# Kernel tuning notes

Measured on AMD Instinct MI355X. Metric: run time of the kernel, lower is better.

## Reference

```python
import jax, jax.numpy as jnp
import numpy as np

NV, NC = 100000, 50000        # num variables, num constraints
DV, DC = 8, 16                # padded neighbor-list widths
DIN, DH = 32, 128             # init_input_dim, output_dim (=init_output_dim)
NUM_LAYERS = 3                # aggregate loop runs num_layers-1 times
DCAT = 2 * DH + DIN           # input_dim of fc_variable/fc_constraint


def setup_inputs() -> dict:
    key = jax.random.key(0)
    ks = jax.random.split(key, 10)
    w = lambda k, shape: (jax.random.normal(k, shape, jnp.float32) * 0.05)
    return {
        "x": jax.random.normal(ks[0], (NV + NC, DIN), jnp.float32),
        "var_constr_index": jax.random.randint(ks[1], (NV, DV), 0, NC, dtype=jnp.int32),
        "constr_var_index": jax.random.randint(ks[2], (NC, DC), 0, NV, dtype=jnp.int32),
        "W_init_v": w(ks[3], (DIN, DH)), "b_init_v": jnp.zeros((DH,), jnp.float32),
        "W_init_c": w(ks[4], (DIN, DH)), "b_init_c": jnp.zeros((DH,), jnp.float32),
        "W_var": w(ks[5], (DCAT, DH)), "b_var": jnp.zeros((DH,), jnp.float32),
        "W_con": w(ks[6], (DCAT, DH)), "b_con": jnp.zeros((DH,), jnp.float32),
        "W_q": w(ks[7], (2 * DH, 1)), "b_q": jnp.zeros((1,), jnp.float32),
    }


def reference(x, var_constr_index, constr_var_index,
              W_init_v, b_init_v, W_init_c, b_init_c,
              W_var, b_var, W_con, b_con, W_q, b_q):
    nv = var_constr_index.shape[0]
    xv, xc = x[:nv], x[nv:]
    # layer zero init (fc_init_variables / fc_init_constraints)
    v = xv @ W_init_v + b_init_v          # [NV, DH]
    c = xc @ W_init_c + b_init_c          # [NC, DH]
    # message-passing layers: both updates read OLD v and OLD c
    for _ in range(1, NUM_LAYERS):
        agg_c = jnp.sum(v[constr_var_index], axis=1)   # [NC, DH] gather+sum over variable neighbors
        agg_v = jnp.sum(c[var_constr_index], axis=1)   # [NV, DH] gather+sum over constraint neighbors
        c_new = jnp.concatenate([agg_c, c, xc], axis=1) @ W_con + b_con
        v_new = jnp.concatenate([agg_v, v, xv], axis=1) @ W_var + b_var
        c, v = c_new, v_new
    # embedding_Q: global sum of variable features, broadcast, concat, linear
    g = jnp.sum(v, axis=0)                             # [DH]
    q_in = jnp.concatenate([jnp.broadcast_to(g, v.shape), v], axis=1)  # [NV, 2*DH]
    return q_in @ W_q + b_q                            # [NV, 1]
```

## Files before the change

kernel.cpp:

```cpp
#include <hip/hip_runtime.h>

#define NV 100000
#define NC 50000
#define DVAR 8
#define DCON 16

using short8 = __attribute__((ext_vector_type(8))) short;
using f32x4  = __attribute__((ext_vector_type(4))) float;

__device__ __forceinline__ unsigned short f2bf(float f) {
    union { float f; unsigned int u; } v; v.f = f;
    return (unsigned short)((v.u + 0x7fffu + ((v.u >> 16) & 1u)) >> 16);
}
__device__ __forceinline__ float bflo(unsigned int u) {
    union { unsigned int u; float f; } v; v.u = u << 16; return v.f;
}
__device__ __forceinline__ float bfhi(unsigned int u) {
    union { unsigned int u; float f; } v; v.u = u & 0xffff0000u; return v.f;
}

__global__ __launch_bounds__(256) void pack_kernel(
    const float* __restrict__ Wvar, const float* __restrict__ Wcon,
    const float* __restrict__ Wiv,  const float* __restrict__ Wic,
    unsigned short* __restrict__ WbVar, unsigned short* __restrict__ WbCon,
    unsigned short* __restrict__ WbIv,  unsigned short* __restrict__ WbIc,
    float* __restrict__ S)
{
    const int tid = blockIdx.x * 256 + threadIdx.x;
    for (int i = tid; i < 9 * 128 * 32; i += gridDim.x * 256) {
        int s = i >> 12, rem = i & 4095, c = rem >> 5, k = rem & 31;
        int src = (s * 32 + k) * 128 + c;
        WbVar[i] = f2bf(Wvar[src]);
        WbCon[i] = f2bf(Wcon[src]);
    }
    for (int i = tid; i < 128 * 32; i += gridDim.x * 256) {
        int c = i >> 5, k = i & 31;
        int src = k * 128 + c;
        WbIv[i] = f2bf(Wiv[src]);
        WbIc[i] = f2bf(Wic[src]);
    }
    if (tid == 0) S[0] = 0.f;
}

__global__ __launch_bounds__(256) void init_mfma(
    const float* __restrict__ x,
    const unsigned short* __restrict__ Wb,
    const float* __restrict__ bias,
    unsigned short* __restrict__ hout, int M)
{
    const int t = threadIdx.x;
    const int lane = t & 63;
    const int w = t >> 6;
    const int lrow = lane & 15;
    const int lg = lane >> 4;
    const int wrow0 = blockIdx.x * 64 + w * 16;
    int arow = wrow0 + lrow;
    int arowc = arow < M ? arow : M - 1;

    const float4* xp = (const float4*)(x + (size_t)arowc * 32 + lg * 8);
    float4 xa = xp[0], xb = xp[1];
    short8 afr;
    afr[0] = (short)f2bf(xa.x); afr[1] = (short)f2bf(xa.y);
    afr[2] = (short)f2bf(xa.z); afr[3] = (short)f2bf(xa.w);
    afr[4] = (short)f2bf(xb.x); afr[5] = (short)f2bf(xb.y);
    afr[6] = (short)f2bf(xb.z); afr[7] = (short)f2bf(xb.w);

    #pragma unroll
    for (int ct = 0; ct < 8; ++ct) {
        int c = ct * 16 + lrow;
        short8 bfr = *(const short8*)(Wb + (size_t)c * 32 + lg * 8);
        f32x4 acc = {0.f, 0.f, 0.f, 0.f};
        acc = __builtin_amdgcn_mfma_f32_16x16x32_bf16(afr, bfr, acc, 0, 0, 0);
        float bv = bias[c];
        #pragma unroll
        for (int r = 0; r < 4; ++r) {
            int orow = wrow0 + lg * 4 + r;
            if (orow < M) hout[(size_t)orow * 128 + c] = f2bf(acc[r] + bv);
        }
    }
}

template<int DEG>
__global__ __launch_bounds__(256) void agg_bf16(
    const unsigned short* __restrict__ hnb, const int* __restrict__ idx,
    unsigned short* __restrict__ agg, int M)
{
    const int tid = blockIdx.x * 256 + threadIdx.x;
    const int row = tid >> 4;
    const int part = tid & 15;
    if (row >= M) return;
    int nb[DEG];
    #pragma unroll
    for (int d4 = 0; d4 < DEG / 4; ++d4)
        *(int4*)(&nb[d4 * 4]) = *(const int4*)(idx + (size_t)row * DEG + d4 * 4);
    float a0=0.f,a1=0.f,a2=0.f,a3=0.f,a4=0.f,a5=0.f,a6=0.f,a7=0.f;
    #pragma unroll
    for (int b = 0; b < DEG; b += 8) {
        uint4 q[8];
        #pragma unroll
        for (int j = 0; j < 8; ++j)
            q[j] = *(const uint4*)(hnb + (size_t)nb[b + j] * 128 + part * 8);
        #pragma unroll
        for (int j = 0; j < 8; ++j) {
            a0 += bflo(q[j].x); a1 += bfhi(q[j].x);
            a2 += bflo(q[j].y); a3 += bfhi(q[j].y);
            a4 += bflo(q[j].z); a5 += bfhi(q[j].z);
            a6 += bflo(q[j].w); a7 += bfhi(q[j].w);
        }
    }
    uint4 o;
    o.x = (unsigned)f2bf(a0) | ((unsigned)f2bf(a1) << 16);
    o.y = (unsigned)f2bf(a2) | ((unsigned)f2bf(a3) << 16);
    o.z = (unsigned)f2bf(a4) | ((unsigned)f2bf(a5) << 16);
    o.w = (unsigned)f2bf(a6) | ((unsigned)f2bf(a7) << 16);
    *(uint4*)(agg + (size_t)row * 128 + part * 8) = o;
}

template<bool FINAL>
__global__ __launch_bounds__(256) void gemm_mfma(
    const unsigned short* hself,
    const unsigned short* __restrict__ aggin,
    const float* __restrict__ xself,
    const unsigned short* __restrict__ Wb,
    const float* __restrict__ bias,
    unsigned short* hout,
    const float* __restrict__ Wq, float* __restrict__ S, float* __restrict__ dotout,
    int M)
{
    __shared__ float red[4];
    const int t = threadIdx.x;
    const int lane = t & 63;
    const int w = t >> 6;
    const int lrow = lane & 15;
    const int lg = lane >> 4;
    const int wrow0 = blockIdx.x * 128 + w * 32;

    int arc[2];
    #pragma unroll
    for (int rt = 0; rt < 2; ++rt) {
        int r = wrow0 + rt * 16 + lrow;
        arc[rt] = r < M ? r : M - 1;
    }

    auto loadA = [&](int s, int rt) -> short8 {
        if (s < 4) {
            return *(const short8*)(aggin + (size_t)arc[rt] * 128 + s * 32 + lg * 8);
        } else if (s < 8) {
            return *(const short8*)(hself + (size_t)arc[rt] * 128 + (s - 4) * 32 + lg * 8);
        } else {
            const float4* xp = (const float4*)(xself + (size_t)arc[rt] * 32 + lg * 8);
            float4 xa = xp[0], xb = xp[1];
            short8 r8;
            r8[0] = (short)f2bf(xa.x); r8[1] = (short)f2bf(xa.y);
            r8[2] = (short)f2bf(xa.z); r8[3] = (short)f2bf(xa.w);
            r8[4] = (short)f2bf(xb.x); r8[5] = (short)f2bf(xb.y);
            r8[6] = (short)f2bf(xb.z); r8[7] = (short)f2bf(xb.w);
            return r8;
        }
    };

    short8 bfr[2][8];
    short8 afr[2][2];
    #pragma unroll
    for (int ct = 0; ct < 8; ++ct)
        bfr[0][ct] = *(const short8*)(Wb + ((size_t)(ct * 16 + lrow)) * 32 + lg * 8);
    afr[0][0] = loadA(0, 0);
    afr[0][1] = loadA(0, 1);

    f32x4 acc[2][8];
    #pragma unroll
    for (int rt = 0; rt < 2; ++rt)
        #pragma unroll
        for (int ct = 0; ct < 8; ++ct) acc[rt][ct] = (f32x4){0.f, 0.f, 0.f, 0.f};

    #pragma unroll
    for (int s = 0; s < 9; ++s) {
        const int cur = s & 1, nxt = cur ^ 1;
        if (s < 8) {
            #pragma unroll
            for (int ct = 0; ct < 8; ++ct)
                bfr[nxt][ct] = *(const short8*)(
                    Wb + ((size_t)(s + 1) * 128 + ct * 16 + lrow) * 32 + lg * 8);
            afr[nxt][0] = loadA(s + 1, 0);
            afr[nxt][1] = loadA(s + 1, 1);
        }
        #pragma unroll
        for (int ct = 0; ct < 8; ++ct)
            #pragma unroll
            for (int rt = 0; rt < 2; ++rt)
                acc[rt][ct] = __builtin_amdgcn_mfma_f32_16x16x32_bf16(
                    afr[cur][rt], bfr[cur][ct], acc[rt][ct], 0, 0, 0);
    }

    if (!FINAL) {
        #pragma unroll
        for (int rt = 0; rt < 2; ++rt)
            #pragma unroll
            for (int ct = 0; ct < 8; ++ct) {
                int c = ct * 16 + lrow;
                float bv = bias[c];
                #pragma unroll
                for (int r = 0; r < 4; ++r) {
                    int orow = wrow0 + rt * 16 + lg * 4 + r;
                    if (orow < M) hout[(size_t)orow * 128 + c] = f2bf(acc[rt][ct][r] + bv);
                }
            }
    } else {
        float tot = 0.f;
        #pragma unroll
        for (int rt = 0; rt < 2; ++rt) {
            float d0[4] = {0.f, 0.f, 0.f, 0.f};
            float d1[4] = {0.f, 0.f, 0.f, 0.f};
            #pragma unroll
            for (int ct = 0; ct < 8; ++ct) {
                int c = ct * 16 + lrow;
                float bv = bias[c];
                float wq0 = Wq[c];
                float wq1 = Wq[128 + c];
                #pragma unroll
                for (int r = 0; r < 4; ++r) {
                    int orow = wrow0 + rt * 16 + lg * 4 + r;
                    float val = (orow < M) ? (acc[rt][ct][r] + bv) : 0.f;
                    d0[r] += val * wq0;
                    d1[r] += val * wq1;
                }
            }
            #pragma unroll
            for (int r = 0; r < 4; ++r) {
                d0[r] += __shfl_xor(d0[r], 1); d0[r] += __shfl_xor(d0[r], 2);
                d0[r] += __shfl_xor(d0[r], 4); d0[r] += __shfl_xor(d0[r], 8);
                d1[r] += __shfl_xor(d1[r], 1); d1[r] += __shfl_xor(d1[r], 2);
                d1[r] += __shfl_xor(d1[r], 4); d1[r] += __shfl_xor(d1[r], 8);
            }
            if (lrow == 0) {
                #pragma unroll
                for (int r = 0; r < 4; ++r) {
                    int orow = wrow0 + rt * 16 + lg * 4 + r;
                    if (orow < M) dotout[orow] = d1[r];
                }
            }
            tot += d0[0] + d0[1] + d0[2] + d0[3];
        }
        tot += __shfl_xor(tot, 16);
        tot += __shfl_xor(tot, 32);
        if (lane == 0) red[w] = tot;
        __syncthreads();
        if (t == 0) atomicAdd(S, red[0] + red[1] + red[2] + red[3]);
    }
}

__global__ __launch_bounds__(256) void addout_kernel(
    float* __restrict__ outp, const float* __restrict__ S,
    const float* __restrict__ bq, int n)
{
    int i = blockIdx.x * 256 + threadIdx.x;
    if (i < n) outp[i] = outp[i] + S[0] + bq[0];
}

extern "C" void kernel_launch(void* const* d_in, const int* in_sizes, int n_in,
                              void* d_out, int out_size, void* d_ws, size_t ws_size,
                              hipStream_t stream)
{
    const float* x    = (const float*)d_in[0];
    const int*   vci  = (const int*)  d_in[1];
    const int*   cvi  = (const int*)  d_in[2];
    const float* Wiv  = (const float*)d_in[3];
    const float* biv  = (const float*)d_in[4];
    const float* Wic  = (const float*)d_in[5];
    const float* bic  = (const float*)d_in[6];
    const float* Wvar = (const float*)d_in[7];
    const float* bvar = (const float*)d_in[8];
    const float* Wcon = (const float*)d_in[9];
    const float* bcon = (const float*)d_in[10];
    const float* Wq   = (const float*)d_in[11];
    const float* bq   = (const float*)d_in[12];
    float* outp = (float*)d_out;

    unsigned short* us = (unsigned short*)d_ws;
    size_t o = 0;
    unsigned short* vA    = us + o; o += (size_t)NV * 128;
    unsigned short* cA    = us + o; o += (size_t)NC * 128;
    unsigned short* cB    = us + o; o += (size_t)NC * 128;
    unsigned short* aggV  = us + o; o += (size_t)NV * 128;
    unsigned short* aggC  = us + o; o += (size_t)NC * 128;
    unsigned short* WbVar = us + o; o += 9 * 128 * 32;
    unsigned short* WbCon = us + o; o += 9 * 128 * 32;
    unsigned short* WbIv  = us + o; o += 128 * 32;
    unsigned short* WbIc  = us + o; o += 128 * 32;
    float* S = (float*)(us + o);

    const float* xc = x + (size_t)NV * 32;

    pack_kernel<<<144, 256, 0, stream>>>(Wvar, Wcon, Wiv, Wic, WbVar, WbCon, WbIv, WbIc, S);
    init_mfma<<<(NV + 63) / 64, 256, 0, stream>>>(x,  WbIv, biv, vA, NV);
    init_mfma<<<(NC + 63) / 64, 256, 0, stream>>>(xc, WbIc, bic, cA, NC);

    agg_bf16<DCON><<<(NC * 16 + 255) / 256, 256, 0, stream>>>(vA, cvi, aggC, NC);
    agg_bf16<DVAR><<<(NV * 16 + 255) / 256, 256, 0, stream>>>(cA, vci, aggV, NV);
    gemm_mfma<false><<<(NC + 127) / 128, 256, 0, stream>>>(
        cA, aggC, xc, WbCon, bcon, cB, nullptr, nullptr, nullptr, NC);
    gemm_mfma<false><<<(NV + 127) / 128, 256, 0, stream>>>(
        vA, aggV, x, WbVar, bvar, vA, nullptr, nullptr, nullptr, NV);

    agg_bf16<DVAR><<<(NV * 16 + 255) / 256, 256, 0, stream>>>(cB, vci, aggV, NV);
    gemm_mfma<true><<<(NV + 127) / 128, 256, 0, stream>>>(
        vA, aggV, x, WbVar, bvar, nullptr, Wq, S, outp, NV);

    addout_kernel<<<(NV + 255) / 256, 256, 0, stream>>>(outp, S, bq, NV);
}
```

Before: 297.3 us.

## Double per-wave GEMM row tile to 64 rows and reorder K-loop

Each wave now computes 64 output rows (4 row tiles) instead of 32, so each weight fragment loaded from global memory is reused across twice as many MFMAs and the grid is halved. The x-input K-slice is processed first, outside the main loop, which is restructured into explicit ping-pong A/B register buffers. A launch-bounds occupancy hint of 2 is added. The doubled accumulator array (128 floats per lane) plus the fragment buffers greatly raises register pressure, which risks lower occupancy or spills.

New measurement: 274.0 us. 7.8% less time.

```diff
diff --git a/kernel.cpp b/kernel.cpp
--- a/kernel.cpp
+++ b/kernel.cpp
@@ -117,7 +117,7 @@
 }
 
 template<bool FINAL>
-__global__ __launch_bounds__(256) void gemm_mfma(
+__global__ __launch_bounds__(256, 2) void gemm_mfma(
     const unsigned short* hself,
     const unsigned short* __restrict__ aggin,
     const float* __restrict__ xself,
@@ -133,68 +133,76 @@
     const int w = t >> 6;
     const int lrow = lane & 15;
     const int lg = lane >> 4;
-    const int wrow0 = blockIdx.x * 128 + w * 32;
-
-    int arc[2];
-    #pragma unroll
-    for (int rt = 0; rt < 2; ++rt) {
+    const int wrow0 = blockIdx.x * 256 + w * 64;
+
+    int arc[4];
+    #pragma unroll
+    for (int rt = 0; rt < 4; ++rt) {
         int r = wrow0 + rt * 16 + lrow;
         arc[rt] = r < M ? r : M - 1;
     }
 
-    auto loadA = [&](int s, int rt) -> short8 {
-        if (s < 4) {
-            return *(const short8*)(aggin + (size_t)arc[rt] * 128 + s * 32 + lg * 8);
-        } else if (s < 8) {
-            return *(const short8*)(hself + (size_t)arc[rt] * 128 + (s - 4) * 32 + lg * 8);
-        } else {
+    auto loadB = [&](short8* dst, int s) {
+        #pragma unroll
+        for (int ct = 0; ct < 8; ++ct)
+            dst[ct] = *(const short8*)(Wb + ((size_t)s * 128 + ct * 16 + lrow) * 32 + lg * 8);
+    };
+    auto loadA = [&](short8* dst, int s) {
+        const unsigned short* src = (s < 4) ? aggin : hself;
+        const int off = (s & 3) * 32 + lg * 8;
+        #pragma unroll
+        for (int rt = 0; rt < 4; ++rt)
+            dst[rt] = *(const short8*)(src + (size_t)arc[rt] * 128 + off);
+    };
+
+    f32x4 acc[4][8];
+    short8 bA[8], bB[8], aA[4], aB[4];
+
+    loadB(bA, 8);
+    loadB(bB, 0); loadA(aB, 0);
+    {
+        short8 xfr[4];
+        #pragma unroll
+        for (int rt = 0; rt < 4; ++rt) {
             const float4* xp = (const float4*)(xself + (size_t)arc[rt] * 32 + lg * 8);
             float4 xa = xp[0], xb = xp[1];
-            short8 r8;
-            r8[0] = (short)f2bf(xa.x); r8[1] = (short)f2bf(xa.y);
-            r8[2] = (short)f2bf(xa.z); r8[3] = (short)f2bf(xa.w);
-            r8[4] = (short)f2bf(xb.x); r8[5] = (short)f2bf(xb.y);
-            r8[6] = (short)f2bf(xb.z); r8[7] = (short)f2bf(xb.w);
-            return r8;
-        }
-    };
-
-    short8 bfr[2][8];
-    short8 afr[2][2];
-    #pragma unroll
-    for (int ct = 0; ct < 8; ++ct)
-        bfr[0][ct] = *(const short8*)(Wb + ((size_t)(ct * 16 + lrow)) * 32 + lg * 8);
-    afr[0][0] = loadA(0, 0);
-    afr[0][1] = loadA(0, 1);
-
-    f32x4 acc[2][8];
-    #pragma unroll
-    for (int rt = 0; rt < 2; ++rt)
-        #pragma unroll
-        for (int ct = 0; ct < 8; ++ct) acc[rt][ct] = (f32x4){0.f, 0.f, 0.f, 0.f};
-
-    #pragma unroll
-    for (int s = 0; s < 9; ++s) {
-        const int cur = s & 1, nxt = cur ^ 1;
-        if (s < 8) {
+            xfr[rt][0] = (short)f2bf(xa.x); xfr[rt][1] = (short)f2bf(xa.y);
+            xfr[rt][2] = (short)f2bf(xa.z); xfr[rt][3] = (short)f2bf(xa.w);
+            xfr[rt][4] = (short)f2bf(xb.x); xfr[rt][5] = (short)f2bf(xb.y);
+            xfr[rt][6] = (short)f2bf(xb.z); xfr[rt][7] = (short)f2bf(xb.w);
+        }
+        #pragma unroll
+        for (int ct = 0; ct < 8; ++ct)
+            #pragma unroll
+            for (int rt = 0; rt < 4; ++rt)
+                acc[rt][ct] = __builtin_amdgcn_mfma_f32_16x16x32_bf16(
+                    xfr[rt], bA[ct], (f32x4){0.f, 0.f, 0.f, 0.f}, 0, 0, 0);
+    }
+
+    #pragma unroll
+    for (int k = 0; k < 8; ++k) {
+        if ((k & 1) == 0) {
+            if (k < 7) { loadB(bA, k + 1); loadA(aA, k + 1); }
             #pragma unroll
             for (int ct = 0; ct < 8; ++ct)
-                bfr[nxt][ct] = *(const short8*)(
-                    Wb + ((size_t)(s + 1) * 128 + ct * 16 + lrow) * 32 + lg * 8);
-            afr[nxt][0] = loadA(s + 1, 0);
-            afr[nxt][1] = loadA(s + 1, 1);
-        }
-        #pragma unroll
-        for (int ct = 0; ct < 8; ++ct)
-            #pragma unroll
-            for (int rt = 0; rt < 2; ++rt)
-                acc[rt][ct] = __builtin_amdgcn_mfma_f32_16x16x32_bf16(
-                    afr[cur][rt], bfr[cur][ct], acc[rt][ct], 0, 0, 0);
+                #pragma unroll
+                for (int rt = 0; rt < 4; ++rt)
+                    acc[rt][ct] = __builtin_amdgcn_mfma_f32_16x16x32_bf16(
+                        aB[rt], bB[ct], acc[rt][ct], 0, 0, 0);
+        } else {
+            if (k < 7) { loadB(bB, k + 1); loadA(aB, k + 1); }
+            #pragma unroll
+            for (int ct = 0; ct < 8; ++ct)
+                #pragma unroll
+                for (int rt = 0; rt < 4; ++rt)
+                    acc[rt][ct] = __builtin_amdgcn_mfma_f32_16x16x32_bf16(
+                        aA[rt], bA[ct], acc[rt][ct], 0, 0, 0);
+        }
     }
 
     if (!FINAL) {
         #pragma unroll
-        for (int rt = 0; rt < 2; ++rt)
+        for (int rt = 0; rt < 4; ++rt)
             #pragma unroll
             for (int ct = 0; ct < 8; ++ct) {
                 int c = ct * 16 + lrow;
@@ -208,7 +216,7 @@
     } else {
         float tot = 0.f;
         #pragma unroll
-        for (int rt = 0; rt < 2; ++rt) {
+        for (int rt = 0; rt < 4; ++rt) {
             float d0[4] = {0.f, 0.f, 0.f, 0.f};
             float d1[4] = {0.f, 0.f, 0.f, 0.f};
             #pragma unroll
@@ -297,13 +305,13 @@
 
     agg_bf16<DCON><<<(NC * 16 + 255) / 256, 256, 0, stream>>>(vA, cvi, aggC, NC);
     agg_bf16<DVAR><<<(NV * 16 + 255) / 256, 256, 0, stream>>>(cA, vci, aggV, NV);
-    gemm_mfma<false><<<(NC + 127) / 128, 256, 0, stream>>>(
+    gemm_mfma<false><<<(NC + 255) / 256, 256, 0, stream>>>(
         cA, aggC, xc, WbCon, bcon, cB, nullptr, nullptr, nullptr, NC);
-    gemm_mfma<false><<<(NV + 127) / 128, 256, 0, stream>>>(
+    gemm_mfma<false><<<(NV + 255) / 256, 256, 0, stream>>>(
         vA, aggV, x, WbVar, bvar, vA, nullptr, nullptr, nullptr, NV);
 
     agg_bf16<DVAR><<<(NV * 16 + 255) / 256, 256, 0, stream>>>(cB, vci, aggV, NV);
-    gemm_mfma<true><<<(NV + 127) / 128, 256, 0, stream>>>(
+    gemm_mfma<true><<<(NV + 255) / 256, 256, 0, stream>>>(
         vA, aggV, x, WbVar, bvar, nullptr, Wq, S, outp, NV);
 
     addout_kernel<<<(NV + 255) / 256, 256, 0, stream>>>(outp, S, bq, NV);
```
